# Optimization experiments

Measured on AMD Instinct MI355X. Metric: run time of the kernel, lower is better.

The kernel has to match this reference:

```python
import jax, jax.numpy as jnp
import numpy as np
from jax import lax

DIM = 1024
NUM_HEADS = 16
B, L = 4, 4096


def setup_inputs() -> dict:
    key = jax.random.key(0)
    ks = jax.random.split(key, 7)
    D = DIM // NUM_HEADS
    s = lambda fan_in: 1.0 / np.sqrt(fan_in)
    x = jax.random.normal(ks[0], (B, L, DIM), dtype=jnp.float32)
    w_qk = jax.random.uniform(ks[1], (2 * DIM, DIM), jnp.float32, -s(DIM), s(DIM))
    b_qk = jax.random.uniform(ks[2], (2 * DIM,), jnp.float32, -s(DIM), s(DIM))
    w_v = jax.random.uniform(ks[3], (DIM, DIM), jnp.float32, -s(DIM), s(DIM))
    b_v = jax.random.uniform(ks[4], (DIM,), jnp.float32, -s(DIM), s(DIM))
    # depthwise Conv1d: out_channels=D, in_channels/groups=1, kernel=3
    w_lepe = jax.random.uniform(ks[5], (D, 1, 3), jnp.float32, -s(3), s(3))
    b_lepe = jax.random.uniform(ks[6], (D,), jnp.float32, -s(3), s(3))
    return {"x": x, "w_qk": w_qk, "b_qk": b_qk, "w_v": w_v, "b_v": b_v,
            "w_lepe": w_lepe, "b_lepe": b_lepe, "num_heads": NUM_HEADS}


def _lepe_add(a, w_lepe, b_lepe):
    # a: (B,H,L,D). Faithful to torch: raw reshape (NOT transpose) to (B*H, D, L),
    # depthwise conv over last axis, reshape back to (B,H,D,L), then transpose.
    Bc, H, Lc, D = a.shape
    ar = a.reshape(Bc * H, D, Lc)
    conv = lax.conv_general_dilated(
        ar, w_lepe, window_strides=(1,), padding=((1, 1),),
        feature_group_count=D,
        dimension_numbers=("NCH", "OIH", "NCH"))
    conv = conv + b_lepe[None, :, None]
    return a + conv.reshape(Bc, H, D, Lc).transpose(0, 1, 3, 2)


def reference(x, w_qk, b_qk, w_v, b_v, w_lepe, b_lepe, num_heads):
    Bc, Lc, C = x.shape
    H = num_heads
    D = C // H
    qk = (x @ w_qk.T + b_qk).reshape(Bc, Lc, 2, H, D).transpose(2, 0, 3, 1, 4)
    q, k = qk[0], qk[1]                                  # (B,H,L,D)
    v = (x @ w_v.T + b_v).reshape(Bc, Lc, H, D).transpose(0, 2, 1, 3)
    q = jax.nn.elu(q) + 1.0
    k = jax.nn.elu(k) + 1.0
    q = _lepe_add(q, w_lepe, b_lepe)
    k = _lepe_add(k, w_lepe, b_lepe)
    k_mean = k.mean(axis=2, keepdims=True)               # (B,H,1,D)
    z = 1.0 / (jnp.einsum("bhld,bhmd->bhlm", q, k_mean) + 1e-6)  # (B,H,L,1)
    kv = jnp.einsum("bhld,bhle->bhde", k, v) / Lc        # (B,H,D,D)
    out = jnp.einsum("bhld,bhde->bhle", q, kv) * z       # (B,H,L,D)
    return out.transpose(0, 2, 1, 3).reshape(Bc, Lc, C)
```

## Files before the change

### kernel.cpp

```cpp
#include <hip/hip_runtime.h>
#include <hip/hip_bf16.h>
#include <stdint.h>

typedef __bf16 bf16;
typedef __bf16 bf16x8 __attribute__((ext_vector_type(8)));
typedef __bf16 bf16x4 __attribute__((ext_vector_type(4)));
typedef float  f32x4  __attribute__((ext_vector_type(4)));

static __device__ __forceinline__ void gll16(const void* g, void* l) {
    __builtin_amdgcn_global_load_lds((__attribute__((address_space(1))) void*)(void*)g,
                                     (__attribute__((address_space(3))) void*)l, 16, 0, 0);
}

__global__ __launch_bounds__(256) void cvt_f32_bf16(const float* __restrict__ in,
                                                    bf16* __restrict__ out, int n4) {
    int i = blockIdx.x * 256 + threadIdx.x;
    const int stride = gridDim.x * 256;
    for (; i < n4; i += stride) {
        f32x4 v = *(const f32x4*)(in + (size_t)i * 4);
        bf16x4 o;
        o[0] = (bf16)v[0]; o[1] = (bf16)v[1]; o[2] = (bf16)v[2]; o[3] = (bf16)v[3];
        *(bf16x4*)(out + (size_t)i * 4) = o;
    }
}

__global__ __launch_bounds__(256) void gemm_qkv(const bf16* __restrict__ X,
                                                const bf16* __restrict__ W,
                                                const float* __restrict__ b_qk,
                                                const float* __restrict__ b_v,
                                                bf16* __restrict__ Y) {
    __shared__ bf16 sm[8192];
    const int t    = threadIdx.x;
    const int lane = t & 63;
    const int wv   = t >> 6;
    const int wr   = wv >> 1, wc = wv & 1;
    const int m0   = blockIdx.x * 128;
    const int n0   = blockIdx.y * 128;

    const int sr = t >> 2;
    const int sc = (t & 3) * 8;
    const bf16* gA0 = X + (size_t)(m0 + sr) * 1024 + sc;
    const bf16* gA1 = gA0 + (size_t)64 * 1024;
    const bf16* gB0 = W + (size_t)(n0 + sr) * 1024 + sc;
    const bf16* gB1 = gB0 + (size_t)64 * 1024;
    char* smb = (char*)sm;
    char* lA0 = smb + t * 16;
    char* lA1 = smb + 4096  + t * 16;
    char* lB0 = smb + 8192  + t * 16;
    char* lB1 = smb + 12288 + t * 16;

    const bf16* As = sm;
    const bf16* Bs = sm + 4096;
    const int fr = lane & 15;
    const int fk = (lane >> 4) * 8;

    f32x4 acc[4][4] = {};

    for (int k0 = 0; k0 < 1024; k0 += 32) {
        gll16(gA0 + k0, lA0);
        gll16(gA1 + k0, lA1);
        gll16(gB0 + k0, lB0);
        gll16(gB1 + k0, lB1);
        __syncthreads();
        bf16x8 aF[4], bF[4];
#pragma unroll
        for (int mi = 0; mi < 4; ++mi)
            aF[mi] = *(const bf16x8*)(As + (wr * 64 + mi * 16 + fr) * 32 + fk);
#pragma unroll
        for (int ni = 0; ni < 4; ++ni)
            bF[ni] = *(const bf16x8*)(Bs + (wc * 64 + ni * 16 + fr) * 32 + fk);
#pragma unroll
        for (int mi = 0; mi < 4; ++mi)
#pragma unroll
            for (int ni = 0; ni < 4; ++ni)
                acc[mi][ni] = __builtin_amdgcn_mfma_f32_16x16x32_bf16(aF[mi], bF[ni], acc[mi][ni], 0, 0, 0);
        __syncthreads();
    }

    const bool isqk = (n0 < 2048);
#pragma unroll
    for (int ni = 0; ni < 4; ++ni) {
        const int col = n0 + wc * 64 + ni * 16 + (lane & 15);
        const float bv = isqk ? b_qk[col] : b_v[col - 2048];
#pragma unroll
        for (int mi = 0; mi < 4; ++mi) {
            const int row0 = m0 + wr * 64 + mi * 16 + (lane >> 4) * 4;
#pragma unroll
            for (int j = 0; j < 4; ++j) {
                float vo = acc[mi][ni][j] + bv;
                if (isqk) vo = vo > 0.f ? vo + 1.f : expf(vo);
                Y[(size_t)(row0 + j) * 3072 + col] = (bf16)vo;
            }
        }
    }
}

__global__ __launch_bounds__(256) void lepe(const bf16* __restrict__ Y,
                                            const float* __restrict__ wl,
                                            const float* __restrict__ bl,
                                            bf16* __restrict__ qf,
                                            bf16* __restrict__ kf) {
    const int bx = blockIdx.x;
    const int bh = bx >> 6, m = bx & 63;
    const int b = bh >> 4, h = bh & 15;
    const int isK = blockIdx.y;
    const bf16* slab = Y + (size_t)(b * 4096) * 3072 + isK * 1024 + h * 64;
    bf16* outp = (isK ? kf : qf) + (size_t)(b * 4096) * 1024 + h * 64;

    __shared__ bf16  Gs[64][72];
    __shared__ float Cs[64][65];
    __shared__ float ep[64], en[64];
    const int t = threadIdx.x;
    {
        const int d = t >> 2, c0 = (t & 3) * 16;
        const bf16* src = slab + (size_t)(d * 64 + m) * 3072 + c0;
        *(bf16x8*)&Gs[d][c0]     = *(const bf16x8*)src;
        *(bf16x8*)&Gs[d][c0 + 8] = *(const bf16x8*)(src + 8);
    }
    if (t < 64) {
        const int d = t;
        ep[d] = (m > 0)  ? (float)slab[(size_t)(d * 64 + m - 1) * 3072 + 63] : 0.f;
        en[d] = (m < 63) ? (float)slab[(size_t)(d * 64 + m + 1) * 3072 + 0]  : 0.f;
    }
    __syncthreads();
    {
        const int d = t >> 2, j0 = (t & 3) * 16;
        const float w0 = wl[d * 3], w1 = wl[d * 3 + 1], w2 = wl[d * 3 + 2], bb = bl[d];
#pragma unroll
        for (int jj = 0; jj < 16; ++jj) {
            const int j = j0 + jj;
            const float left  = (j == 0)  ? ep[d] : (float)Gs[d][j - 1];
            const float mid   = (float)Gs[d][j];
            const float right = (j == 63) ? en[d] : (float)Gs[d][j + 1];
            Cs[d][j] = w0 * left + w1 * mid + w2 * right + bb;
        }
    }
    __syncthreads();
    {
        const int j = t >> 2, c0 = (t & 3) * 16;
        const size_t l = (size_t)(m * 64 + j);
        const bf16* arow = slab + l * 3072 + c0;
        bf16* orow = outp + l * 1024 + c0;
        bf16x8 a0 = *(const bf16x8*)arow;
        bf16x8 a1 = *(const bf16x8*)(arow + 8);
        bf16x8 o0, o1;
#pragma unroll
        for (int i = 0; i < 8; ++i) {
            o0[i] = (bf16)((float)a0[i] + Cs[c0 + i][j]);
            o1[i] = (bf16)((float)a1[i] + Cs[c0 + 8 + i][j]);
        }
        *(bf16x8*)orow = o0;
        *(bf16x8*)(orow + 8) = o1;
    }
}

__global__ __launch_bounds__(256) void kv_partial(const bf16* __restrict__ kf,
                                                  const bf16* __restrict__ Y,
                                                  float* __restrict__ kvp,
                                                  float* __restrict__ ksp) {
    const int bh = blockIdx.x, ch = blockIdx.y;
    const int b = bh >> 4, h = bh & 15;
    const bf16* K = kf + (size_t)(b * 4096) * 1024 + h * 64;
    const bf16* V = Y + (size_t)(b * 4096) * 3072 + 2048 + h * 64;
    __shared__ float Ks[16][64];
    __shared__ float Vs[16][64];
    const int t = threadIdx.x;
    const int d = t >> 2, e0 = (t & 3) * 16;
    float acc[16] = {};
    float ks = 0.f;
    const int l0 = ch * 1024;
    for (int base = l0; base < l0 + 1024; base += 16) {
        __syncthreads();
        if (t < 128) {
            const int r = t >> 3, s = (t & 7) * 8;
            bf16x8 v = *(const bf16x8*)(K + (size_t)(base + r) * 1024 + s);
#pragma unroll
            for (int i = 0; i < 8; ++i) Ks[r][s + i] = (float)v[i];
        } else {
            const int tt = t - 128, r = tt >> 3, s = (tt & 7) * 8;
            bf16x8 v = *(const bf16x8*)(V + (size_t)(base + r) * 3072 + s);
#pragma unroll
            for (int i = 0; i < 8; ++i) Vs[r][s + i] = (float)v[i];
        }
        __syncthreads();
#pragma unroll
        for (int ll = 0; ll < 16; ++ll) {
            const float kd = Ks[ll][d];
            ks += kd;
            const float* vr = &Vs[ll][e0];
#pragma unroll
            for (int e = 0; e < 16; ++e) acc[e] += kd * vr[e];
        }
    }
    float* o = kvp + (((size_t)ch * 64 + bh) * 64 + d) * 64 + e0;
#pragma unroll
    for (int e = 0; e < 16; ++e) o[e] = acc[e];
    if (e0 == 0) ksp[(size_t)ch * 4096 + bh * 64 + d] = ks;
}

__global__ __launch_bounds__(256) void out_kernel(const bf16* __restrict__ qf,
                                                  const float* __restrict__ kvp,
                                                  const float* __restrict__ ksp,
                                                  float* __restrict__ out) {
    const int bh = blockIdx.x;
    const int b = bh >> 4, h = bh & 15;
    __shared__ float kvS[4096];
    __shared__ float ksS[64];
    const int t = threadIdx.x;
    const float* kp = kvp + (size_t)bh * 4096;
#pragma unroll
    for (int i = 0; i < 4; ++i) {
        const int idx = i * 1024 + t * 4;
        f32x4 v = *(const f32x4*)(kp + idx);
        v = v + *(const f32x4*)(kp + 262144 + idx);
        v = v + *(const f32x4*)(kp + 524288 + idx);
        v = v + *(const f32x4*)(kp + 786432 + idx);
        *(f32x4*)(kvS + idx) = v;
    }
    if (t < 64) {
        ksS[t] = ksp[bh * 64 + t] + ksp[4096 + bh * 64 + t] +
                 ksp[8192 + bh * 64 + t] + ksp[12288 + bh * 64 + t];
    }
    __syncthreads();

    const int l = blockIdx.y * 256 + t;
    const size_t row = (size_t)(b * 4096 + l);
    const bf16* qrow = qf + row * 1024 + h * 64;
    bf16x8 qv[8];
#pragma unroll
    for (int i = 0; i < 8; ++i) qv[i] = *(const bf16x8*)(qrow + i * 8);

    float s = 0.f;
#pragma unroll
    for (int i = 0; i < 8; ++i)
#pragma unroll
        for (int j = 0; j < 8; ++j) s += (float)qv[i][j] * ksS[i * 8 + j];
    const float inv = 1.0f / (s + 0.004096f);

    f32x4 acc[16] = {};
#pragma unroll
    for (int i = 0; i < 8; ++i) {
#pragma unroll
        for (int j = 0; j < 8; ++j) {
            const float qd = (float)qv[i][j];
            const float* kr = kvS + (i * 8 + j) * 64;
#pragma unroll
            for (int e4 = 0; e4 < 16; ++e4)
                acc[e4] += qd * (*(const f32x4*)(kr + e4 * 4));
        }
    }
    float* orow = out + row * 1024 + h * 64;
#pragma unroll
    for (int e4 = 0; e4 < 16; ++e4) {
        *(f32x4*)(orow + e4 * 4) = acc[e4] * inv;
    }
}

extern "C" void kernel_launch(void* const* d_in, const int* in_sizes, int n_in,
                              void* d_out, int out_size, void* d_ws, size_t ws_size,
                              hipStream_t stream) {
    const float* x      = (const float*)d_in[0];
    const float* w_qk   = (const float*)d_in[1];
    const float* b_qk   = (const float*)d_in[2];
    const float* w_v    = (const float*)d_in[3];
    const float* b_v    = (const float*)d_in[4];
    const float* w_lepe = (const float*)d_in[5];
    const float* b_lepe = (const float*)d_in[6];

    char* ws = (char*)d_ws;
    bf16*  Y   = (bf16*)ws;
    bf16*  xb  = (bf16*)(ws + 100663296);
    bf16*  Wb  = (bf16*)(ws + 134217728);
    float* kvp = (float*)(ws + 167772160);
    float* ksp = (float*)(ws + 171966464);
    bf16* qf = xb;
    bf16* kf = Wb;

    cvt_f32_bf16<<<2048, 256, 0, stream>>>(x, xb, 16777216 / 4);
    cvt_f32_bf16<<<512,  256, 0, stream>>>(w_qk, Wb, 2097152 / 4);
    cvt_f32_bf16<<<256,  256, 0, stream>>>(w_v, Wb + 2097152, 1048576 / 4);
    gemm_qkv<<<dim3(128, 24), 256, 0, stream>>>(xb, Wb, b_qk, b_v, Y);
    lepe<<<dim3(4096, 2), 256, 0, stream>>>(Y, w_lepe, b_lepe, qf, kf);
    kv_partial<<<dim3(64, 4), 256, 0, stream>>>(kf, Y, kvp, ksp);
    out_kernel<<<dim3(64, 16), 256, 0, stream>>>(qf, kvp, ksp, (float*)d_out);
}
```

Before: 479.8 us.

## Register-tile kv_partial and out_kernel with prefetch and split-wave reduction

kv_partial now loads 64-row K/V tiles into padded LDS using vectorized float4 stores. The next tile's global loads are issued before the compute loop so they overlap with it. Each wave accumulates an 8x8 outer-product register tile over its 16 rows, and the four waves' partials are reduced through LDS. out_kernel assigns 4 rows x 16 columns per thread so each kv row read from LDS is reused across 4 query rows, cutting LDS traffic per FMA. The cost is higher register pressure and extra reduction synchronization.

```diff
diff --git a/kernel.cpp b/kernel.cpp
--- a/kernel.cpp
+++ b/kernel.cpp
@@ -162,40 +162,125 @@
     const int b = bh >> 4, h = bh & 15;
     const bf16* K = kf + (size_t)(b * 4096) * 1024 + h * 64;
     const bf16* V = Y + (size_t)(b * 4096) * 3072 + 2048 + h * 64;
-    __shared__ float Ks[16][64];
-    __shared__ float Vs[16][64];
+
+    __shared__ float SM[64 * 68 * 2 + 4 * 64];
+#define KS(r, c) SM[(r) * 68 + (c)]
+#define VS(r, c) SM[4352 + (r) * 68 + (c)]
+    float* ksr = SM + 8704;
+
     const int t = threadIdx.x;
-    const int d = t >> 2, e0 = (t & 3) * 16;
-    float acc[16] = {};
-    float ks = 0.f;
+    const int lane = t & 63;
+    const int w = t >> 6;
+    const int dg = lane >> 3, eg = lane & 7;
+
+    f32x4 acc[8][2] = {};
+    f32x4 ks0 = {}, ks1 = {};
+
+    const int j = t >> 2, c0 = (t & 3) * 16;
     const int l0 = ch * 1024;
-    for (int base = l0; base < l0 + 1024; base += 16) {
+    const bf16* Kp = K + (size_t)(l0 + j) * 1024 + c0;
+    const bf16* Vp = V + (size_t)(l0 + j) * 3072 + c0;
+    bf16x8 k0 = *(const bf16x8*)Kp, k1 = *(const bf16x8*)(Kp + 8);
+    bf16x8 v0 = *(const bf16x8*)Vp, v1 = *(const bf16x8*)(Vp + 8);
+
+    for (int s = 0; s < 16; ++s) {
         __syncthreads();
-        if (t < 128) {
-            const int r = t >> 3, s = (t & 7) * 8;
-            bf16x8 v = *(const bf16x8*)(K + (size_t)(base + r) * 1024 + s);
-#pragma unroll
-            for (int i = 0; i < 8; ++i) Ks[r][s + i] = (float)v[i];
-        } else {
-            const int tt = t - 128, r = tt >> 3, s = (tt & 7) * 8;
-            bf16x8 v = *(const bf16x8*)(V + (size_t)(base + r) * 3072 + s);
-#pragma unroll
-            for (int i = 0; i < 8; ++i) Vs[r][s + i] = (float)v[i];
+        {
+            f32x4 a, bx, c, d2;
+#pragma unroll
+            for (int i = 0; i < 4; ++i) { a[i] = (float)k0[i]; bx[i] = (float)k0[4 + i]; }
+            *(f32x4*)&KS(j, c0) = a;  *(f32x4*)&KS(j, c0 + 4) = bx;
+#pragma unroll
+            for (int i = 0; i < 4; ++i) { c[i] = (float)k1[i]; d2[i] = (float)k1[4 + i]; }
+            *(f32x4*)&KS(j, c0 + 8) = c; *(f32x4*)&KS(j, c0 + 12) = d2;
+#pragma unroll
+            for (int i = 0; i < 4; ++i) { a[i] = (float)v0[i]; bx[i] = (float)v0[4 + i]; }
+            *(f32x4*)&VS(j, c0) = a;  *(f32x4*)&VS(j, c0 + 4) = bx;
+#pragma unroll
+            for (int i = 0; i < 4; ++i) { c[i] = (float)v1[i]; d2[i] = (float)v1[4 + i]; }
+            *(f32x4*)&VS(j, c0 + 8) = c; *(f32x4*)&VS(j, c0 + 12) = d2;
         }
         __syncthreads();
-#pragma unroll
-        for (int ll = 0; ll < 16; ++ll) {
-            const float kd = Ks[ll][d];
-            ks += kd;
-            const float* vr = &Vs[ll][e0];
-#pragma unroll
-            for (int e = 0; e < 16; ++e) acc[e] += kd * vr[e];
-        }
-    }
-    float* o = kvp + (((size_t)ch * 64 + bh) * 64 + d) * 64 + e0;
-#pragma unroll
-    for (int e = 0; e < 16; ++e) o[e] = acc[e];
-    if (e0 == 0) ksp[(size_t)ch * 4096 + bh * 64 + d] = ks;
+        if (s < 15) {
+            Kp += (size_t)64 * 1024; Vp += (size_t)64 * 3072;
+            k0 = *(const bf16x8*)Kp; k1 = *(const bf16x8*)(Kp + 8);
+            v0 = *(const bf16x8*)Vp; v1 = *(const bf16x8*)(Vp + 8);
+        }
+#pragma unroll
+        for (int jj = 0; jj < 16; ++jj) {
+            const int l = w * 16 + jj;
+            f32x4 ka = *(const f32x4*)&KS(l, dg * 8);
+            f32x4 kb = *(const f32x4*)&KS(l, dg * 8 + 4);
+            f32x4 va = *(const f32x4*)&VS(l, eg * 8);
+            f32x4 vb = *(const f32x4*)&VS(l, eg * 8 + 4);
+            ks0 += ka; ks1 += kb;
+#pragma unroll
+            for (int i = 0; i < 4; ++i) {
+                acc[i][0] += ka[i] * va;     acc[i][1] += ka[i] * vb;
+                acc[4 + i][0] += kb[i] * va; acc[4 + i][1] += kb[i] * vb;
+            }
+        }
+    }
+
+    __syncthreads();
+    if (eg == 0) {
+#pragma unroll
+        for (int i = 0; i < 4; ++i) {
+            ksr[w * 64 + dg * 8 + i]     = ks0[i];
+            ksr[w * 64 + dg * 8 + 4 + i] = ks1[i];
+        }
+    }
+    if (w == 1 || w == 3) {
+        float* buf = SM + (w >> 1) * 4352 + lane * 68;
+#pragma unroll
+        for (int i = 0; i < 8; ++i) {
+            *(f32x4*)(buf + i * 8) = acc[i][0];
+            *(f32x4*)(buf + i * 8 + 4) = acc[i][1];
+        }
+    }
+    __syncthreads();
+    if (w == 0 || w == 2) {
+        float* buf = SM + (w >> 1) * 4352 + lane * 68;
+#pragma unroll
+        for (int i = 0; i < 8; ++i) {
+            acc[i][0] += *(const f32x4*)(buf + i * 8);
+            acc[i][1] += *(const f32x4*)(buf + i * 8 + 4);
+        }
+    }
+    __syncthreads();
+    if (w == 2) {
+        float* buf = SM + lane * 68;
+#pragma unroll
+        for (int i = 0; i < 8; ++i) {
+            *(f32x4*)(buf + i * 8) = acc[i][0];
+            *(f32x4*)(buf + i * 8 + 4) = acc[i][1];
+        }
+    }
+    __syncthreads();
+    if (w == 0) {
+        float* buf = SM + lane * 68;
+#pragma unroll
+        for (int i = 0; i < 8; ++i) {
+            acc[i][0] += *(const f32x4*)(buf + i * 8);
+            acc[i][1] += *(const f32x4*)(buf + i * 8 + 4);
+        }
+        float* o = kvp + (((size_t)ch * 64 + bh) * 64 + dg * 8) * 64 + eg * 8;
+#pragma unroll
+        for (int i = 0; i < 8; ++i) {
+            *(f32x4*)(o + (size_t)i * 64)     = acc[i][0];
+            *(f32x4*)(o + (size_t)i * 64 + 4) = acc[i][1];
+        }
+        if (eg == 0) {
+#pragma unroll
+            for (int i = 0; i < 8; ++i) {
+                const int d = dg * 8 + i;
+                ksp[(size_t)ch * 4096 + bh * 64 + d] =
+                    ksr[d] + ksr[64 + d] + ksr[128 + d] + ksr[192 + d];
+            }
+        }
+    }
+#undef KS
+#undef VS
 }
 
 __global__ __launch_bounds__(256) void out_kernel(const bf16* __restrict__ qf,
@@ -223,36 +308,52 @@
     }
     __syncthreads();
 
-    const int l = blockIdx.y * 256 + t;
-    const size_t row = (size_t)(b * 4096 + l);
-    const bf16* qrow = qf + row * 1024 + h * 64;
-    bf16x8 qv[8];
-#pragma unroll
-    for (int i = 0; i < 8; ++i) qv[i] = *(const bf16x8*)(qrow + i * 8);
-
-    float s = 0.f;
-#pragma unroll
-    for (int i = 0; i < 8; ++i)
-#pragma unroll
-        for (int j = 0; j < 8; ++j) s += (float)qv[i][j] * ksS[i * 8 + j];
-    const float inv = 1.0f / (s + 0.004096f);
-
-    f32x4 acc[16] = {};
-#pragma unroll
-    for (int i = 0; i < 8; ++i) {
-#pragma unroll
-        for (int j = 0; j < 8; ++j) {
-            const float qd = (float)qv[i][j];
-            const float* kr = kvS + (i * 8 + j) * 64;
-#pragma unroll
-            for (int e4 = 0; e4 < 16; ++e4)
-                acc[e4] += qd * (*(const f32x4*)(kr + e4 * 4));
-        }
-    }
-    float* orow = out + row * 1024 + h * 64;
-#pragma unroll
-    for (int e4 = 0; e4 < 16; ++e4) {
-        *(f32x4*)(orow + e4 * 4) = acc[e4] * inv;
+    const int rg = t >> 2, eg = t & 3, e0 = eg * 16;
+    const int r0 = blockIdx.y * 256 + rg * 4;
+    const bf16* qbase = qf + (size_t)(b * 4096 + r0) * 1024 + h * 64;
+
+    bf16x8 qv[4][8];
+#pragma unroll
+    for (int i = 0; i < 4; ++i)
+#pragma unroll
+        for (int s = 0; s < 8; ++s)
+            qv[i][s] = *(const bf16x8*)(qbase + (size_t)i * 1024 + s * 8);
+
+    float inv[4];
+#pragma unroll
+    for (int i = 0; i < 4; ++i) {
+        float s = 0.f;
+#pragma unroll
+        for (int ss = 0; ss < 8; ++ss)
+#pragma unroll
+            for (int jj = 0; jj < 8; ++jj)
+                s += (float)qv[i][ss][jj] * ksS[ss * 8 + jj];
+        inv[i] = 1.0f / (s + 0.004096f);
+    }
+
+    f32x4 acc[4][4] = {};
+#pragma unroll
+    for (int d = 0; d < 64; ++d) {
+        const float* kr = kvS + d * 64 + e0;
+        f32x4 k0 = *(const f32x4*)kr;
+        f32x4 k1 = *(const f32x4*)(kr + 4);
+        f32x4 k2 = *(const f32x4*)(kr + 8);
+        f32x4 k3 = *(const f32x4*)(kr + 12);
+#pragma unroll
+        for (int i = 0; i < 4; ++i) {
+            const float qd = (float)qv[i][d >> 3][d & 7];
+            acc[i][0] += qd * k0;
+            acc[i][1] += qd * k1;
+            acc[i][2] += qd * k2;
+            acc[i][3] += qd * k3;
+        }
+    }
+#pragma unroll
+    for (int i = 0; i < 4; ++i) {
+        float* orow = out + (size_t)(b * 4096 + r0 + i) * 1024 + h * 64 + e0;
+#pragma unroll
+        for (int q = 0; q < 4; ++q)
+            *(f32x4*)(orow + q * 4) = acc[i][q] * inv[i];
     }
 }
 
```

Measured after the change: 423.5 us. 1.13x faster.
